# Kernel tuning notes

Hardware: AMD Instinct MI355X
Metric: run time of the kernel (lower is better)

Reference implementation:

```python
import jax, jax.numpy as jnp
import numpy as np


def setup_inputs() -> dict:
    key = jax.random.key(0)
    ks = jax.random.split(key, 4)
    B, T, D, U = 64, 2048, 256, 256
    x = jax.random.normal(ks[0], (B, T, D), dtype=jnp.float32)
    s = 1.0 / np.sqrt(D)
    kz = jax.random.normal(ks[1], (D, U), dtype=jnp.float32) * s
    kr = jax.random.normal(ks[2], (D, U), dtype=jnp.float32) * s
    kh = jax.random.normal(ks[3], (D, U), dtype=jnp.float32) * s
    return {
        'x': x, 'kz': kz, 'kr': kr, 'kh': kh,
        'mz': jnp.ones((U,), jnp.float32), 'mr': jnp.ones((U,), jnp.float32),
        'bz': jnp.zeros((U,), jnp.float32), 'br': jnp.zeros((U,), jnp.float32),
        'bh': jnp.zeros((U,), jnp.float32),
    }


def reference(x, kz, kr, kh, mz, mr, bz, br, bh):
    # Precompute the three input projections for all timesteps (batched GEMMs),
    # then scan the purely elementwise recurrence over time.
    xz = jnp.einsum('btd,du->btu', x, kz) + bz  # [B,T,U]
    xr = jnp.einsum('btd,du->btu', x, kr) + br
    xh = jnp.einsum('btd,du->btu', x, kh) + bh
    B, T, U = xz.shape
    h0 = jnp.zeros((B, U), x.dtype)

    def step(h, inp):
        xz_t, xr_t, xh_t = inp
        r = jnp.tanh(xr_t + h * mr) + 1.0
        z = jax.nn.sigmoid(xz_t + h * mz)
        hh = jnp.tanh(xh_t + r * h)
        out = (1.0 - z) * hh + z * h
        return out, out

    # scan over time axis: move T to leading axis
    xs = (jnp.swapaxes(xz, 0, 1), jnp.swapaxes(xr, 0, 1), jnp.swapaxes(xh, 0, 1))
    _, ys = jax.lax.scan(step, h0, xs)
    return jnp.swapaxes(ys, 0, 1)  # [B,T,U]
```

## Files before the change

### kernel.cpp

```cpp
#include <hip/hip_runtime.h>
#include <hip/hip_bf16.h>

#define BB 64
#define TT 2048
#define DD 256
#define UU 256
#define MM (BB*TT)
#define NN (3*UU)
#define PLANE ((size_t)BB*TT*UU)

typedef _Float16 half8 __attribute__((ext_vector_type(8)));
typedef _Float16 half4 __attribute__((ext_vector_type(4)));
typedef float floatx4 __attribute__((ext_vector_type(4)));

__device__ inline float fexp2(float x){
#if __has_builtin(__builtin_amdgcn_exp2f)
  return __builtin_amdgcn_exp2f(x);
#else
  return exp2f(x);
#endif
}
__device__ inline float frcp(float x){
#if __has_builtin(__builtin_amdgcn_rcpf)
  return __builtin_amdgcn_rcpf(x);
#else
  return 1.0f/x;
#endif
}
__device__ inline float ftanh(float a){
  const float TWO_L2E = 2.8853900817779268f;
  return 1.0f - 2.0f*frcp(fexp2(TWO_L2E*a) + 1.0f);
}
__device__ inline float fsigmoid(float a){
  const float L2E = 1.4426950408889634f;
  return frcp(1.0f + fexp2(-L2E*a));
}

__global__ __launch_bounds__(256) void prep_kernel(const float* __restrict__ kz,
                                                   const float* __restrict__ kr,
                                                   const float* __restrict__ kh,
                                                   _Float16* __restrict__ K16T){
  int o = blockIdx.x*256 + threadIdx.x;
  int n = o >> 8;
  int k = o & 255;
  int p = n >> 8;
  int u = n & 255;
  const float* w = (p==0) ? kz : ((p==1) ? kr : kh);
  K16T[o] = (_Float16)w[k*UU + u];
}

#define BM 128
#define BN 128
#define BK 32
#define LDA 40

__global__ __launch_bounds__(256) void gemm_kernel(const float* __restrict__ X,
                                                   const _Float16* __restrict__ K16T,
                                                   const float* __restrict__ bz,
                                                   const float* __restrict__ br,
                                                   const float* __restrict__ bh,
                                                   _Float16* __restrict__ P){
  __shared__ __align__(16) _Float16 As[BM*LDA];
  __shared__ __align__(16) _Float16 Bs[BN*BK];
  const int tid = threadIdx.x;
  const int bx = blockIdx.x;
  const int by = blockIdx.y;
  const int rowBase = by*BM;
  const int nBase = bx*BN;

  const int wave = tid >> 6, lane = tid & 63;
  const int wm = wave & 1, wn = wave >> 1;
  const int lrow = lane & 15, lkq = lane >> 4;

  floatx4 acc[4][4] = {};

  const int arow = tid >> 1;
  const int acol = (tid & 1) * 16;
  const float* aptr = X + (size_t)(rowBase + arow)*DD + acol;
  _Float16* asdst = &As[arow*LDA + acol];

  for (int k0 = 0; k0 < DD; k0 += BK) {
    __syncthreads();
    #pragma unroll
    for (int i = 0; i < 2; i++) {
      int c = i*256 + tid;
      const _Float16* g = K16T + (size_t)(nBase + (c>>2))*DD + k0 + (c&3)*8;
      __builtin_amdgcn_global_load_lds(
          (const __attribute__((address_space(1))) void*)g,
          (__attribute__((address_space(3))) void*)(Bs + c*8),
          16, 0, 0);
    }
    floatx4 a0 = *(const floatx4*)(aptr + k0);
    floatx4 a1 = *(const floatx4*)(aptr + k0 + 4);
    floatx4 a2 = *(const floatx4*)(aptr + k0 + 8);
    floatx4 a3 = *(const floatx4*)(aptr + k0 + 12);
    half8 pk0, pk1;
    #pragma unroll
    for (int q = 0; q < 4; q++){
      pk0[q]   = (_Float16)a0[q];
      pk0[4+q] = (_Float16)a1[q];
      pk1[q]   = (_Float16)a2[q];
      pk1[4+q] = (_Float16)a3[q];
    }
    *(half8*)asdst       = pk0;
    *(half8*)(asdst + 8) = pk1;
    __syncthreads();
    half8 af[4], bf[4];
    #pragma unroll
    for (int i = 0; i < 4; i++)
      af[i] = *(const half8*)&As[(wm*64 + i*16 + lrow)*LDA + lkq*8];
    #pragma unroll
    for (int j = 0; j < 4; j++)
      bf[j] = *(const half8*)&Bs[(wn*64 + j*16 + lrow)*BK + lkq*8];
    #pragma unroll
    for (int i = 0; i < 4; i++)
      #pragma unroll
      for (int j = 0; j < 4; j++)
        acc[i][j] = __builtin_amdgcn_mfma_f32_16x16x32_f16(af[i], bf[j], acc[i][j], 0, 0, 0);
  }

  const int p = bx >> 1;
  const int ub = (bx & 1) * 128;
  const float* bias = (p==0) ? bz : ((p==1) ? br : bh);
  _Float16* Pp = P + (size_t)p * PLANE;
  const int bidx = rowBase >> 11;
  const int t0 = (rowBase & 2047) + wm*64 + lkq*4;
  #pragma unroll
  for (int j = 0; j < 4; j++){
    int col = ub + wn*64 + j*16 + lrow;
    float bv = bias[col];
    _Float16* rowp = Pp + (size_t)(bidx*UU + col)*TT + t0;
    #pragma unroll
    for (int i = 0; i < 4; i++){
      half4 v;
      #pragma unroll
      for (int r = 0; r < 4; r++)
        v[r] = (_Float16)(acc[i][j][r] + bv);
      *(half4*)(rowp + i*16) = v;
    }
  }
}

#define PF 16
#define NBUF 4
__global__ __launch_bounds__(64) void scan_kernel(const _Float16* __restrict__ P,
                                                  const float* __restrict__ mz,
                                                  const float* __restrict__ mr,
                                                  float* __restrict__ out){
  const int ci = blockIdx.x*64 + threadIdx.x;
  const int b = ci >> 8;
  const int u = ci & 255;
  const half8* pz = (const half8*)(P + (size_t)ci*TT);
  const half8* pr = (const half8*)(P + PLANE + (size_t)ci*TT);
  const half8* ph = (const half8*)(P + 2*PLANE + (size_t)ci*TT);
  float* po = out + (size_t)b*(TT*UU) + u;
  const float vmz = mz[u], vmr = mr[u];
  float h = 0.0f;

  half8 qz[NBUF][2], qr[NBUF][2], qh[NBUF][2];

#define LOADC(buf, c) do { \
    qz[buf][0] = pz[(c)*2];   qz[buf][1] = pz[(c)*2+1]; \
    qr[buf][0] = pr[(c)*2];   qr[buf][1] = pr[(c)*2+1]; \
    qh[buf][0] = ph[(c)*2];   qh[buf][1] = ph[(c)*2+1]; \
  } while(0)

#define PROC(buf, c) do { \
    _Pragma("unroll") \
    for (int i = 0; i < PF; i++){ \
      float xz = (float)qz[buf][i>>3][i&7]; \
      float xr = (float)qr[buf][i>>3][i&7]; \
      float xh = (float)qh[buf][i>>3][i&7]; \
      float r  = ftanh(xr + h*vmr) + 1.0f; \
      float z  = fsigmoid(xz + h*vmz); \
      float hh = ftanh(xh + r*h); \
      h = (1.0f - z)*hh + z*h; \
      po[(size_t)((c)*PF + i)*UU] = h; \
    } \
    if ((c) + NBUF < NC) LOADC(buf, (c) + NBUF); \
  } while(0)

  const int NC = TT/PF;
  LOADC(0, 0); LOADC(1, 1); LOADC(2, 2); LOADC(3, 3);
  for (int c = 0; c < NC; c += NBUF){
    PROC(0, c);
    PROC(1, c+1);
    PROC(2, c+2);
    PROC(3, c+3);
  }
#undef LOADC
#undef PROC
}

extern "C" void kernel_launch(void* const* d_in, const int* in_sizes, int n_in,
                              void* d_out, int out_size, void* d_ws, size_t ws_size,
                              hipStream_t stream) {
  (void)in_sizes; (void)n_in; (void)out_size; (void)ws_size;
  const float* x  = (const float*)d_in[0];
  const float* kz = (const float*)d_in[1];
  const float* kr = (const float*)d_in[2];
  const float* kh = (const float*)d_in[3];
  const float* mz = (const float*)d_in[4];
  const float* mr = (const float*)d_in[5];
  const float* bz = (const float*)d_in[6];
  const float* br = (const float*)d_in[7];
  const float* bh = (const float*)d_in[8];
  float* out = (float*)d_out;

  _Float16* K16T = (_Float16*)d_ws;
  _Float16* P    = (_Float16*)((char*)d_ws + 393216);

  hipLaunchKernelGGL(prep_kernel, dim3(NN*DD/256), dim3(256), 0, stream, kz, kr, kh, K16T);
  hipLaunchKernelGGL(gemm_kernel, dim3(NN/BN, MM/BM), dim3(256), 0, stream,
                     x, K16T, bz, br, bh, P);
  hipLaunchKernelGGL(scan_kernel, dim3(256), dim3(64), 0, stream, P, mz, mr, out);
}
```

Before: 467.2 us.

## Swizzle GEMM B tile in LDS and restructure scan recurrence math

The GEMM now XOR-swizzles the k-quarter index of the B tile, both when loading it into LDS and when reading it back, to cut LDS bank conflicts on the fragment reads. The scan kernel converts each chunk of inputs to float ahead of time and issues the next prefetch before the dependent loop. It also rewrites the gate math with fused multiply-adds to shorten the serial dependency chain per timestep, and switches pointer arithmetic to 32-bit offsets. The 32-bit offsets carry a small overflow risk but stay in range for these sizes.

```diff
diff --git a/kernel.cpp b/kernel.cpp
--- a/kernel.cpp
+++ b/kernel.cpp
@@ -26,14 +26,6 @@
 #else
   return 1.0f/x;
 #endif
-}
-__device__ inline float ftanh(float a){
-  const float TWO_L2E = 2.8853900817779268f;
-  return 1.0f - 2.0f*frcp(fexp2(TWO_L2E*a) + 1.0f);
-}
-__device__ inline float fsigmoid(float a){
-  const float L2E = 1.4426950408889634f;
-  return frcp(1.0f + fexp2(-L2E*a));
 }
 
 __global__ __launch_bounds__(256) void prep_kernel(const float* __restrict__ kz,
@@ -71,6 +63,7 @@
   const int wave = tid >> 6, lane = tid & 63;
   const int wm = wave & 1, wn = wave >> 1;
   const int lrow = lane & 15, lkq = lane >> 4;
+  const int bsw = (lrow >> 1) & 3;
 
   floatx4 acc[4][4] = {};
 
@@ -84,7 +77,9 @@
     #pragma unroll
     for (int i = 0; i < 2; i++) {
       int c = i*256 + tid;
-      const _Float16* g = K16T + (size_t)(nBase + (c>>2))*DD + k0 + (c&3)*8;
+      int n = c >> 2, kq = c & 3;
+      int kqs = kq ^ ((n >> 1) & 3);
+      const _Float16* g = K16T + (size_t)(nBase + n)*DD + k0 + kqs*8;
       __builtin_amdgcn_global_load_lds(
           (const __attribute__((address_space(1))) void*)g,
           (__attribute__((address_space(3))) void*)(Bs + c*8),
@@ -111,7 +106,7 @@
       af[i] = *(const half8*)&As[(wm*64 + i*16 + lrow)*LDA + lkq*8];
     #pragma unroll
     for (int j = 0; j < 4; j++)
-      bf[j] = *(const half8*)&Bs[(wn*64 + j*16 + lrow)*BK + lkq*8];
+      bf[j] = *(const half8*)&Bs[(wn*64 + j*16 + lrow)*BK + ((lkq ^ bsw)*8)];
     #pragma unroll
     for (int i = 0; i < 4; i++)
       #pragma unroll
@@ -143,18 +138,20 @@
 
 #define PF 16
 #define NBUF 4
-__global__ __launch_bounds__(64) void scan_kernel(const _Float16* __restrict__ P,
-                                                  const float* __restrict__ mz,
-                                                  const float* __restrict__ mr,
-                                                  float* __restrict__ out){
+__global__ __launch_bounds__(64, 1) void scan_kernel(const _Float16* __restrict__ P,
+                                                     const float* __restrict__ mz,
+                                                     const float* __restrict__ mr,
+                                                     float* __restrict__ out){
   const int ci = blockIdx.x*64 + threadIdx.x;
   const int b = ci >> 8;
   const int u = ci & 255;
-  const half8* pz = (const half8*)(P + (size_t)ci*TT);
-  const half8* pr = (const half8*)(P + PLANE + (size_t)ci*TT);
-  const half8* ph = (const half8*)(P + 2*PLANE + (size_t)ci*TT);
-  float* po = out + (size_t)b*(TT*UU) + u;
+  const half8* pz = (const half8*)P + ci*(TT/8);
+  const half8* pr = (const half8*)(P + PLANE) + ci*(TT/8);
+  const half8* ph = (const half8*)(P + 2*PLANE) + ci*(TT/8);
+  float* po = out + b*(TT*UU) + u;
   const float vmz = mz[u], vmr = mr[u];
+  const float TWO_L2E = 2.8853900817779268f;
+  const float NL2E    = -1.4426950408889634f;
   float h = 0.0f;
 
   half8 qz[NBUF][2], qr[NBUF][2], qh[NBUF][2];
@@ -166,18 +163,28 @@
   } while(0)
 
 #define PROC(buf, c) do { \
+    float fz[PF], fr[PF], fh[PF]; \
     _Pragma("unroll") \
     for (int i = 0; i < PF; i++){ \
-      float xz = (float)qz[buf][i>>3][i&7]; \
-      float xr = (float)qr[buf][i>>3][i&7]; \
-      float xh = (float)qh[buf][i>>3][i&7]; \
-      float r  = ftanh(xr + h*vmr) + 1.0f; \
-      float z  = fsigmoid(xz + h*vmz); \
-      float hh = ftanh(xh + r*h); \
-      h = (1.0f - z)*hh + z*h; \
-      po[(size_t)((c)*PF + i)*UU] = h; \
+      fz[i] = (float)qz[buf][i>>3][i&7]; \
+      fr[i] = (float)qr[buf][i>>3][i&7]; \
+      fh[i] = (float)qh[buf][i>>3][i&7]; \
     } \
     if ((c) + NBUF < NC) LOADC(buf, (c) + NBUF); \
+    const int toff = (c)*PF*UU; \
+    _Pragma("unroll") \
+    for (int i = 0; i < PF; i++){ \
+      float ar = fmaf(h, vmr, fr[i]); \
+      float Er = fexp2(TWO_L2E*ar); \
+      float r  = fmaf(-2.0f, frcp(Er + 1.0f), 2.0f);    \
+      float az = fmaf(h, vmz, fz[i]); \
+      float z  = frcp(1.0f + fexp2(NL2E*az));           \
+      float ah = fmaf(r, h, fh[i]); \
+      float Eh = fexp2(TWO_L2E*ah); \
+      float th = fmaf(-2.0f, frcp(Eh + 1.0f), 1.0f);    \
+      h = fmaf(z, h - th, th); \
+      po[toff + i*UU] = h; \
+    } \
   } while(0)
 
   const int NC = TT/PF;
```

Result: no change. 473.1 us (+1.3%).
